# Performance work log

Measured on AMD Instinct MI355X. Metric: run time of the kernel, lower is better.

Reference implementation:

```python
import jax, jax.numpy as jnp
import numpy as np

N_TARGETS = 4
BATCH_SIZE = 4
B = N_TARGETS * BATCH_SIZE
N_SAMPLES = 1024
LAYERS = [(128, 128), (256, 64), (512, 32)]  # (channels, spatial)
EPS_COS = 1e-10


def setup_inputs() -> dict:
    key = jax.random.key(0)
    inp = {}
    for l, (c, s) in enumerate(LAYERS):
        k1, k2, k3, k4, key = jax.random.split(key, 5)
        n = s * s
        inp[f't{l}'] = jax.random.normal(k1, (N_TARGETS, c, s, s), dtype=jnp.float32)
        inp[f'g{l}'] = jax.random.normal(k2, (B, c, s, s), dtype=jnp.float32)
        inp[f'ix{l}'] = jax.random.randint(k3, (B, N_SAMPLES), 0, n)
        inp[f'iy{l}'] = jax.random.randint(k4, (B, N_SAMPLES), 0, n)
    return inp


def _cos_remd(x, y):
    # x: (b,n,c), y: (b,m,c)
    xn = jnp.linalg.norm(x, axis=2, keepdims=True)            # (b,n,1)
    yn = jnp.linalg.norm(y, axis=2, keepdims=True)            # (b,m,1)
    cross = jnp.einsum('bnc,bmc->bnm', x, y)                  # (b,n,m)
    dist = 1.0 - cross / (xn * yn.transpose(0, 2, 1) + EPS_COS)
    m1 = dist.min(axis=1).mean(axis=1)                        # min over n, mean over m
    m2 = dist.min(axis=2).mean(axis=1)                        # min over m, mean over n
    return jnp.maximum(m1, m2)                                # (b,)


def _moment_loss(x, y):
    mu_x = x.mean(axis=1, keepdims=True)
    mu_y = y.mean(axis=1, keepdims=True)
    mu_diff = jnp.abs(mu_x - mu_y).mean(axis=(1, 2))
    x_c = x - mu_x
    y_c = y - mu_y
    x_cov = jnp.einsum('bnc,bnd->bcd', x_c, x_c) / (x.shape[1] - 1)
    y_cov = jnp.einsum('bmc,bmd->bcd', y_c, y_c) / (y.shape[1] - 1)
    cov_diff = jnp.abs(x_cov - y_cov).mean(axis=(1, 2))
    return mu_diff + cov_diff                                 # (b,)


def _layer_loss(t, g, ix, iy):
    b, c, h, w = g.shape
    y = jnp.tile(t, (BATCH_SIZE, 1, 1, 1)).reshape(b, t.shape[1], -1)  # (b,c,n_y)
    x = g.reshape(b, c, -1)                                            # (b,c,n_x)
    x = jnp.take_along_axis(x, ix[:, None, :], axis=2)                 # (b,c,ns)
    y = jnp.take_along_axis(y, iy[:, None, :], axis=2)                 # (b,c,ns)
    x = x.transpose(0, 2, 1)
    y = y.transpose(0, 2, 1)
    return _cos_remd(x, y) + _moment_loss(x, y)


def reference(t0, g0, t1, g1, t2, g2, ix0, iy0, ix1, iy1, ix2, iy2):
    loss = (_layer_loss(t0, g0, ix0, iy0)
            + _layer_loss(t1, g1, ix1, iy1)
            + _layer_loss(t2, g2, ix2, iy2))
    return loss.reshape(BATCH_SIZE, N_TARGETS).mean(axis=0)   # (n_targets,)
```

## Files before the change

kernel.cpp:

```cpp
#include <hip/hip_runtime.h>
#include <math.h>

#define NT 4
#define BSZ 4
#define BB 16
#define NS 1024
#define GCH 4096
#define MAXL 3

typedef unsigned short u16;
typedef __attribute__((ext_vector_type(8))) short bf16x8;
typedef __attribute__((ext_vector_type(4))) float f32x4;

struct LayerP {
    const float *g, *t;
    const int *ix, *iy;
    u16 *Xt, *Yt, *Xs, *Ys;
    float *xp, *yp;
    float *rxn, *ryn;
    float *sx, *sy;
    unsigned *m1u, *m2u;
    float *cov;
    int C, n, nchunk, ntri, lid;
};
struct Tab {
    LayerP L[MAXL];
    int nl, nb, b0, ysh;
    float* losspart;
};

__device__ __forceinline__ unsigned fenc(float f) {
    unsigned u = __float_as_uint(f);
    return (u & 0x80000000u) ? ~u : (u | 0x80000000u);
}
__device__ __forceinline__ float fdec(unsigned u) {
    unsigned v = (u & 0x80000000u) ? (u & 0x7FFFFFFFu) : ~u;
    return __uint_as_float(v);
}
__device__ __forceinline__ u16 f2bf(float f) {
    unsigned u = __float_as_uint(f);
    unsigned r = u + 0x7FFFu + ((u >> 16) & 1u);
    return (u16)(r >> 16);
}
__device__ __forceinline__ float bf2f(u16 h) {
    return __uint_as_float((unsigned)h << 16);
}

__global__ __launch_bounds__(256) void gather_x(Tab tab)
{
    int x = blockIdx.x, l = 0;
    while (l < MAXL - 1 && x >= tab.L[l].C) { x -= tab.L[l].C; ++l; }
    const LayerP P = tab.L[l];
    int c = x, bl = blockIdx.y, bg = tab.b0 + bl;
    int tid = threadIdx.x;
    const float* __restrict__ grow = P.g + ((size_t)bg * P.C + c) * P.n;
    const int* __restrict__ ixr = P.ix + bg * NS;
    __shared__ __align__(16) float buf[GCH];
    __shared__ float red[4];
    int px[4];
    float xv[4] = {0.f, 0.f, 0.f, 0.f};
    #pragma unroll
    for (int r = 0; r < 4; ++r) px[r] = ixr[tid + r * 256];
    int n = P.n;
    for (int lo = 0; lo < n; lo += GCH) {
        int sz = min(GCH, n - lo);
        __syncthreads();
        for (int i = tid * 4; i < sz; i += 1024)
            *(float4*)&buf[i] = *(const float4*)&grow[lo + i];
        __syncthreads();
        #pragma unroll
        for (int r = 0; r < 4; ++r) {
            int rel = px[r] - lo;
            if ((unsigned)rel < (unsigned)sz) xv[r] = buf[rel];
        }
    }
    u16* __restrict__ xo = P.Xt + ((size_t)bl * P.C + c) * NS;
    float ax = 0.f;
    #pragma unroll
    for (int r = 0; r < 4; ++r) {
        u16 hb = f2bf(xv[r]);
        xo[tid + r * 256] = hb;
        ax += bf2f(hb);
    }
    for (int o = 32; o > 0; o >>= 1) ax += __shfl_down(ax, o);
    int wid = tid >> 6, lane = tid & 63;
    if (lane == 0) red[wid] = ax;
    __syncthreads();
    if (tid == 0) P.sx[bl * P.C + c] = red[0] + red[1] + red[2] + red[3];
}

__global__ __launch_bounds__(256) void gather_y(Tab tab)
{
    int x = blockIdx.x, l = 0;
    while (l < MAXL - 1 && x >= tab.L[l].C) { x -= tab.L[l].C; ++l; }
    const LayerP P = tab.L[l];
    int c = x, grp = blockIdx.y;
    int tid = threadIdx.x;
    int nk, tgt, bls[4];
    if (tab.ysh == NT) {
        nk = 4; tgt = grp;
        #pragma unroll
        for (int k = 0; k < 4; ++k) bls[k] = grp + NT * k;
    } else {
        nk = 1; bls[0] = grp; tgt = (tab.b0 + grp) % NT;
        bls[1] = bls[2] = bls[3] = 0;
    }
    const float* __restrict__ trow = P.t + ((size_t)tgt * P.C + c) * P.n;
    __shared__ __align__(16) float buf[GCH];
    __shared__ float red[4][4];
    int py[4][4];
    float yv[4][4];
    #pragma unroll
    for (int k = 0; k < 4; ++k) {
        if (k < nk) {
            const int* iyr = P.iy + (tab.b0 + bls[k]) * NS;
            #pragma unroll
            for (int r = 0; r < 4; ++r) { py[k][r] = iyr[tid + r * 256]; yv[k][r] = 0.f; }
        }
    }
    int n = P.n;
    for (int lo = 0; lo < n; lo += GCH) {
        int sz = min(GCH, n - lo);
        __syncthreads();
        for (int i = tid * 4; i < sz; i += 1024)
            *(float4*)&buf[i] = *(const float4*)&trow[lo + i];
        __syncthreads();
        #pragma unroll
        for (int k = 0; k < 4; ++k)
            if (k < nk) {
                #pragma unroll
                for (int r = 0; r < 4; ++r) {
                    int rel = py[k][r] - lo;
                    if ((unsigned)rel < (unsigned)sz) yv[k][r] = buf[rel];
                }
            }
    }
    int wid = tid >> 6, lane = tid & 63;
    #pragma unroll
    for (int k = 0; k < 4; ++k) {
        if (k >= nk) break;
        u16* __restrict__ yo = P.Yt + ((size_t)bls[k] * P.C + c) * NS;
        float ay = 0.f;
        #pragma unroll
        for (int r = 0; r < 4; ++r) {
            u16 hb = f2bf(yv[k][r]);
            yo[tid + r * 256] = hb;
            ay += bf2f(hb);
        }
        for (int o = 32; o > 0; o >>= 1) ay += __shfl_down(ay, o);
        if (lane == 0) red[k][wid] = ay;
    }
    __syncthreads();
    if (tid < nk)
        P.sy[bls[tid] * P.C + c] = red[tid][0] + red[tid][1] + red[tid][2] + red[tid][3];
}

__global__ void transpose_k(Tab tab)
{
    int x = blockIdx.x, l = 0;
    while (l < MAXL - 1 && x >= tab.L[l].C / 64) { x -= tab.L[l].C / 64; ++l; }
    const LayerP P = tab.L[l];
    int z = blockIdx.z;
    int bl = z >> 1, which = z & 1;
    const u16* __restrict__ Zt = which ? P.Yt : P.Xt;
    u16* __restrict__ Zs = which ? P.Ys : P.Xs;
    float* __restrict__ zp = which ? P.yp : P.xp;
    int C = P.C;
    int ctile = x;
    int c0 = ctile * 64, s0 = blockIdx.y * 64;
    __shared__ __align__(16) u16 T[64][72];
    int tid = threadIdx.x;
    #pragma unroll
    for (int rep = 0; rep < 2; ++rep) {
        int q = tid + rep * 256;
        int rr = q >> 3, seg = q & 7;
        *(float4*)&T[rr][seg * 8] =
            *(const float4*)&Zt[((size_t)bl * C + c0 + rr) * NS + s0 + seg * 8];
    }
    __syncthreads();
    #pragma unroll
    for (int rep = 0; rep < 2; ++rep) {
        int q = tid + rep * 256;
        int sr = q >> 3, cs = q & 7;
        __align__(16) u16 tmp[8];
        float p = 0.f;
        #pragma unroll
        for (int e = 0; e < 8; ++e) {
            u16 h = T[cs * 8 + e][sr];
            tmp[e] = h;
            float v = bf2f(h);
            p = fmaf(v, v, p);
        }
        *(float4*)&Zs[((size_t)bl * NS + s0 + sr) * C + c0 + cs * 8] = *(float4*)tmp;
        p += __shfl_xor(p, 1);
        p += __shfl_xor(p, 2);
        p += __shfl_xor(p, 4);
        if (cs == 0)
            zp[((size_t)bl * P.nchunk + ctile) * NS + s0 + sr] = p;
    }
}

__global__ void colnorm_reduce(Tab tab)
{
    const LayerP P = tab.L[blockIdx.y];
    int bl = blockIdx.z;
    int s = blockIdx.x * 256 + threadIdx.x;
    float ax = 0.f, ay = 0.f;
    for (int k = 0; k < P.nchunk; ++k) {
        size_t o = ((size_t)bl * P.nchunk + k) * NS + s;
        ax += P.xp[o];
        ay += P.yp[o];
    }
    P.rxn[bl * NS + s] = rsqrtf(ax);
    P.ryn[bl * NS + s] = rsqrtf(ay);
    P.m1u[bl * NS + s] = 0xFFFFFFFFu;
    P.m2u[bl * NS + s] = 0xFFFFFFFFu;
}

__global__ __launch_bounds__(256) void cross_mfma(Tab tab)
{
    int z = blockIdx.z;
    int l = z / tab.nb, bl = z - l * tab.nb;
    const LayerP P = tab.L[l];
    int C = P.C;
    int i0 = blockIdx.x * 128, j0 = blockIdx.y * 128;
    __shared__ __align__(16) u16 As[128][40], Bs[128][40];
    int tid = threadIdx.x;
    int w = tid >> 6, lane = tid & 63;
    int wr = w >> 1, wc = w & 1;
    int q = lane >> 4, r = lane & 15;
    const u16* __restrict__ Xb = P.Xs + ((size_t)bl * NS + i0) * C;
    const u16* __restrict__ Yb = P.Ys + ((size_t)bl * NS + j0) * C;
    f32x4 acc[4][4];
    #pragma unroll
    for (int m = 0; m < 4; ++m)
        #pragma unroll
        for (int nn = 0; nn < 4; ++nn) acc[m][nn] = (f32x4){0.f, 0.f, 0.f, 0.f};

    for (int kk = 0; kk < C; kk += 32) {
        __syncthreads();
        #pragma unroll
        for (int rep = 0; rep < 2; ++rep) {
            int qid = tid + rep * 256;
            int row = qid >> 2, seg = qid & 3;
            size_t off = (size_t)row * C + kk + seg * 8;
            *(float4*)&As[row][seg * 8] = *(const float4*)&Xb[off];
            *(float4*)&Bs[row][seg * 8] = *(const float4*)&Yb[off];
        }
        __syncthreads();
        bf16x8 a[4], b[4];
        #pragma unroll
        for (int m = 0; m < 4; ++m)
            a[m] = *(const bf16x8*)&As[wr * 64 + m * 16 + r][q * 8];
        #pragma unroll
        for (int nn = 0; nn < 4; ++nn)
            b[nn] = *(const bf16x8*)&Bs[wc * 64 + nn * 16 + r][q * 8];
        #pragma unroll
        for (int m = 0; m < 4; ++m)
            #pragma unroll
            for (int nn = 0; nn < 4; ++nn)
                acc[m][nn] = __builtin_amdgcn_mfma_f32_16x16x32_bf16(a[m], b[nn], acc[m][nn], 0, 0, 0);
    }

    float rxl[4][4], ryl[4];
    #pragma unroll
    for (int m = 0; m < 4; ++m)
        #pragma unroll
        for (int reg = 0; reg < 4; ++reg)
            rxl[m][reg] = P.rxn[bl * NS + i0 + wr * 64 + m * 16 + q * 4 + reg];
    #pragma unroll
    for (int nn = 0; nn < 4; ++nn)
        ryl[nn] = P.ryn[bl * NS + j0 + wc * 64 + nn * 16 + r];

    float rm[4][4], cm[4];
    #pragma unroll
    for (int m = 0; m < 4; ++m)
        #pragma unroll
        for (int reg = 0; reg < 4; ++reg) rm[m][reg] = 1e30f;
    #pragma unroll
    for (int nn = 0; nn < 4; ++nn) cm[nn] = 1e30f;
    #pragma unroll
    for (int m = 0; m < 4; ++m)
        #pragma unroll
        for (int nn = 0; nn < 4; ++nn)
            #pragma unroll
            for (int reg = 0; reg < 4; ++reg) {
                float d = 1.f - acc[m][nn][reg] * rxl[m][reg] * ryl[nn];
                rm[m][reg] = fminf(rm[m][reg], d);
                cm[nn] = fminf(cm[nn], d);
            }
    #pragma unroll
    for (int m = 0; m < 4; ++m)
        #pragma unroll
        for (int reg = 0; reg < 4; ++reg) {
            float v = rm[m][reg];
            v = fminf(v, __shfl_xor(v, 1));
            v = fminf(v, __shfl_xor(v, 2));
            v = fminf(v, __shfl_xor(v, 4));
            v = fminf(v, __shfl_xor(v, 8));
            rm[m][reg] = v;
        }
    if (r == 0) {
        #pragma unroll
        for (int m = 0; m < 4; ++m)
            #pragma unroll
            for (int reg = 0; reg < 4; ++reg) {
                int i = i0 + wr * 64 + m * 16 + q * 4 + reg;
                atomicMin(&P.m2u[bl * NS + i], fenc(rm[m][reg]));
            }
    }
    #pragma unroll
    for (int nn = 0; nn < 4; ++nn) {
        float v = cm[nn];
        v = fminf(v, __shfl_xor(v, 16));
        v = fminf(v, __shfl_xor(v, 32));
        cm[nn] = v;
    }
    if (q == 0) {
        #pragma unroll
        for (int nn = 0; nn < 4; ++nn) {
            int j = j0 + wc * 64 + nn * 16 + r;
            atomicMin(&P.m1u[bl * NS + j], fenc(cm[nn]));
        }
    }
}

__global__ __launch_bounds__(256) void cov_mfma(Tab tab)
{
    int x = blockIdx.x, l = 0;
    while (l < MAXL - 1 && x >= tab.L[l].ntri) { x -= tab.L[l].ntri; ++l; }
    const LayerP P = tab.L[l];
    int u = x;
    int bl = blockIdx.y;
    int C = P.C;
    int ty = 0;
    while ((ty + 1) * (ty + 2) / 2 <= u) ++ty;
    int tx = u - ty * (ty + 1) / 2;
    int c0 = ty * 128, d0 = tx * 128;
    float wgt = (tx == ty) ? 1.f : 2.f;

    __shared__ __align__(16) u16 As[128][40], Bs[128][40], Cs2[128][40], Ds[128][40];
    int tid = threadIdx.x;
    int w = tid >> 6, lane = tid & 63;
    int wr = w >> 1, wc = w & 1;
    int q = lane >> 4, r = lane & 15;
    const u16* __restrict__ Xc = P.Xt + ((size_t)bl * C + c0) * NS;
    const u16* __restrict__ Xd = P.Xt + ((size_t)bl * C + d0) * NS;
    const u16* __restrict__ Yc = P.Yt + ((size_t)bl * C + c0) * NS;
    const u16* __restrict__ Yd = P.Yt + ((size_t)bl * C + d0) * NS;

    f32x4 accX[4][4], accY[4][4];
    #pragma unroll
    for (int m = 0; m < 4; ++m)
        #pragma unroll
        for (int nn = 0; nn < 4; ++nn) {
            accX[m][nn] = (f32x4){0.f, 0.f, 0.f, 0.f};
            accY[m][nn] = (f32x4){0.f, 0.f, 0.f, 0.f};
        }

    for (int ss = 0; ss < NS; ss += 32) {
        __syncthreads();
        #pragma unroll
        for (int rep = 0; rep < 2; ++rep) {
            int qid = tid + rep * 256;
            int row = qid >> 2, seg = qid & 3;
            size_t off = (size_t)row * NS + ss + seg * 8;
            *(float4*)&As[row][seg * 8]  = *(const float4*)&Xc[off];
            *(float4*)&Bs[row][seg * 8]  = *(const float4*)&Xd[off];
            *(float4*)&Cs2[row][seg * 8] = *(const float4*)&Yc[off];
            *(float4*)&Ds[row][seg * 8]  = *(const float4*)&Yd[off];
        }
        __syncthreads();
        {
            bf16x8 a[4], b[4];
            #pragma unroll
            for (int m = 0; m < 4; ++m) a[m] = *(const bf16x8*)&As[wr * 64 + m * 16 + r][q * 8];
            #pragma unroll
            for (int nn = 0; nn < 4; ++nn) b[nn] = *(const bf16x8*)&Bs[wc * 64 + nn * 16 + r][q * 8];
            #pragma unroll
            for (int m = 0; m < 4; ++m)
                #pragma unroll
                for (int nn = 0; nn < 4; ++nn)
                    accX[m][nn] = __builtin_amdgcn_mfma_f32_16x16x32_bf16(a[m], b[nn], accX[m][nn], 0, 0, 0);
        }
        {
            bf16x8 a[4], b[4];
            #pragma unroll
            for (int m = 0; m < 4; ++m) a[m] = *(const bf16x8*)&Cs2[wr * 64 + m * 16 + r][q * 8];
            #pragma unroll
            for (int nn = 0; nn < 4; ++nn) b[nn] = *(const bf16x8*)&Ds[wc * 64 + nn * 16 + r][q * 8];
            #pragma unroll
            for (int m = 0; m < 4; ++m)
                #pragma unroll
                for (int nn = 0; nn < 4; ++nn)
                    accY[m][nn] = __builtin_amdgcn_mfma_f32_16x16x32_bf16(a[m], b[nn], accY[m][nn], 0, 0, 0);
        }
    }

    float scxv[4][4], scyv[4][4], sdxv[4], sdyv[4];
    #pragma unroll
    for (int m = 0; m < 4; ++m)
        #pragma unroll
        for (int reg = 0; reg < 4; ++reg) {
            int c = c0 + wr * 64 + m * 16 + q * 4 + reg;
            scxv[m][reg] = P.sx[bl * C + c];
            scyv[m][reg] = P.sy[bl * C + c];
        }
    #pragma unroll
    for (int nn = 0; nn < 4; ++nn) {
        int d = d0 + wc * 64 + nn * 16 + r;
        sdxv[nn] = P.sx[bl * C + d];
        sdyv[nn] = P.sy[bl * C + d];
    }
    const float invNS = 1.f / NS, invNSm1 = 1.f / (NS - 1);
    float tsum = 0.f;
    #pragma unroll
    for (int m = 0; m < 4; ++m)
        #pragma unroll
        for (int nn = 0; nn < 4; ++nn)
            #pragma unroll
            for (int reg = 0; reg < 4; ++reg) {
                float cx = (accX[m][nn][reg] - scxv[m][reg] * sdxv[nn] * invNS) * invNSm1;
                float cy = (accY[m][nn][reg] - scyv[m][reg] * sdyv[nn] * invNS) * invNSm1;
                tsum += fabsf(cx - cy);
            }
    tsum *= wgt;
    __shared__ float redc[4];
    for (int o = 32; o > 0; o >>= 1) tsum += __shfl_down(tsum, o);
    if (lane == 0) redc[w] = tsum;
    __syncthreads();
    if (tid == 0)
        P.cov[(size_t)bl * P.ntri + u] = redc[0] + redc[1] + redc[2] + redc[3];
}

__global__ void finalize_kernel(Tab tab)
{
    const LayerP P = tab.L[blockIdx.x];
    int bl = blockIdx.y;
    int tid = threadIdx.x;
    int C = P.C;
    float s1 = 0.f, s2 = 0.f, smu = 0.f, scov = 0.f;
    for (int s = tid; s < NS; s += 256) {
        s1 += fdec(P.m1u[bl * NS + s]);
        s2 += fdec(P.m2u[bl * NS + s]);
    }
    for (int c = tid; c < C; c += 256) smu += fabsf(P.sx[bl * C + c] - P.sy[bl * C + c]);
    for (int i = tid; i < P.ntri; i += 256) scov += P.cov[(size_t)bl * P.ntri + i];
    __shared__ float red[4][4];
    for (int o = 32; o > 0; o >>= 1) {
        s1 += __shfl_down(s1, o);
        s2 += __shfl_down(s2, o);
        smu += __shfl_down(smu, o);
        scov += __shfl_down(scov, o);
    }
    int wid = tid >> 6, lane = tid & 63;
    if (lane == 0) { red[0][wid] = s1; red[1][wid] = s2; red[2][wid] = smu; red[3][wid] = scov; }
    __syncthreads();
    if (tid == 0) {
        s1 = red[0][0] + red[0][1] + red[0][2] + red[0][3];
        s2 = red[1][0] + red[1][1] + red[1][2] + red[1][3];
        smu = red[2][0] + red[2][1] + red[2][2] + red[2][3];
        scov = red[3][0] + red[3][1] + red[3][2] + red[3][3];
        float m1m = s1 * (1.f / NS), m2m = s2 * (1.f / NS);
        float mu_diff = smu * (1.f / NS) * (1.f / (float)C);
        float cov_diff = scov / ((float)C * (float)C);
        tab.losspart[(tab.b0 + bl) * 3 + P.lid] = fmaxf(m1m, m2m) + mu_diff + cov_diff;
    }
}

__global__ void out_kernel(const float* __restrict__ lp, float* __restrict__ out)
{
    int t = threadIdx.x;
    if (t < NT) {
        float s = 0.f;
        for (int k = 0; k < BSZ; ++k)
            for (int l = 0; l < 3; ++l)
                s += lp[(k * NT + t) * 3 + l];
        out[t] = s * (1.f / BSZ);
    }
}

static inline size_t alignup(size_t v) { return (v + 255) & ~(size_t)255; }

static size_t layer_bytes(int C, int nb) {
    int nchunk = C / 64;
    int tc = C / 128, ntri = tc * (tc + 1) / 2;
    size_t szZ = alignup((size_t)NS * C * 2);
    size_t szP = alignup((size_t)nchunk * NS * 4);
    return (size_t)nb * (4 * szZ + 2 * szP + 4 * alignup(NS * 4)
                         + 2 * alignup(C * 4) + alignup(ntri * 4));
}

static char* fill_layer(LayerP& P, char* p, int C, int n, int nb, int lid,
                        const float* g, const float* t, const int* ix, const int* iy) {
    P.g = g; P.t = t; P.ix = ix; P.iy = iy;
    P.C = C; P.n = n; P.lid = lid;
    P.nchunk = C / 64;
    int tc = C / 128;
    P.ntri = tc * (tc + 1) / 2;
    size_t szZ = alignup((size_t)NS * C * 2);
    size_t szP = alignup((size_t)P.nchunk * NS * 4);
    P.Xt = (u16*)p;  p += nb * szZ;
    P.Yt = (u16*)p;  p += nb * szZ;
    P.Xs = (u16*)p;  p += nb * szZ;
    P.Ys = (u16*)p;  p += nb * szZ;
    P.xp = (float*)p; p += nb * szP;
    P.yp = (float*)p; p += nb * szP;
    P.rxn = (float*)p; p += nb * alignup(NS * 4);
    P.ryn = (float*)p; p += nb * alignup(NS * 4);
    P.m1u = (unsigned*)p; p += nb * alignup(NS * 4);
    P.m2u = (unsigned*)p; p += nb * alignup(NS * 4);
    P.sx = (float*)p; p += nb * alignup(C * 4);
    P.sy = (float*)p; p += nb * alignup(C * 4);
    P.cov = (float*)p; p += nb * alignup(P.ntri * 4);
    return p;
}

static void launch_group(const Tab& tab, hipStream_t stream) {
    int sumC = 0, sumC64 = 0, sumNtri = 0;
    for (int l = 0; l < tab.nl; ++l) {
        sumC += tab.L[l].C;
        sumC64 += tab.L[l].C / 64;
        sumNtri += tab.L[l].ntri;
    }
    int nb = tab.nb;
    int ygrid = (tab.ysh == NT) ? NT : nb;
    gather_x<<<dim3(sumC, nb), 256, 0, stream>>>(tab);
    gather_y<<<dim3(sumC, ygrid), 256, 0, stream>>>(tab);
    transpose_k<<<dim3(sumC64, NS / 64, nb * 2), 256, 0, stream>>>(tab);
    colnorm_reduce<<<dim3(NS / 256, tab.nl, nb), 256, 0, stream>>>(tab);
    cross_mfma<<<dim3(NS / 128, NS / 128, tab.nl * nb), 256, 0, stream>>>(tab);
    cov_mfma<<<dim3(sumNtri, nb), 256, 0, stream>>>(tab);
    finalize_kernel<<<dim3(tab.nl, nb), 256, 0, stream>>>(tab);
}

extern "C" void kernel_launch(void* const* d_in, const int* in_sizes, int n_in,
                              void* d_out, int out_size, void* d_ws, size_t ws_size,
                              hipStream_t stream)
{
    const float* tp[3] = {(const float*)d_in[0], (const float*)d_in[4], (const float*)d_in[8]};
    const float* gp[3] = {(const float*)d_in[1], (const float*)d_in[5], (const float*)d_in[9]};
    const int* ixp[3]  = {(const int*)d_in[2], (const int*)d_in[6], (const int*)d_in[10]};
    const int* iyp[3]  = {(const int*)d_in[3], (const int*)d_in[7], (const int*)d_in[11]};
    const int Cs[3] = {128, 256, 512};
    const int Sp[3] = {128, 64, 32};

    float* out = (float*)d_out;
    char* ws = (char*)d_ws;
    float* losspart = (float*)ws;
    size_t base = alignup(BB * 3 * 4);
    size_t avail = (ws_size > base) ? ws_size - base : 0;

    size_t need_all = 0;
    for (int l = 0; l < 3; ++l) need_all += layer_bytes(Cs[l], BB);

    if (avail >= need_all) {
        Tab tab;
        tab.nl = 3; tab.nb = BB; tab.b0 = 0; tab.ysh = NT; tab.losspart = losspart;
        char* p = ws + base;
        for (int l = 0; l < 3; ++l)
            p = fill_layer(tab.L[l], p, Cs[l], Sp[l] * Sp[l], BB, l,
                           gp[l], tp[l], ixp[l], iyp[l]);
        launch_group(tab, stream);
    } else {
        for (int l = 0; l < 3; ++l) {
            size_t per_b = layer_bytes(Cs[l], 1);
            int G = (int)(avail / per_b);
            if (G > BB) G = BB;
            if (G < 1) G = 1;
            for (int b0 = 0; b0 < BB; b0 += G) {
                int nb = (BB - b0 < G) ? (BB - b0) : G;
                Tab tab;
                tab.nl = 1; tab.nb = nb; tab.b0 = b0; tab.ysh = 1; tab.losspart = losspart;
                fill_layer(tab.L[0], ws + base, Cs[l], Sp[l] * Sp[l], nb, l,
                           gp[l], tp[l], ixp[l], iyp[l]);
                launch_group(tab, stream);
            }
        }
    }
    out_kernel<<<1, 64, 0, stream>>>(losspart, out);
}
```

Baseline: 230.5 us.

## Pipeline gather row loads via async global-to-LDS quad buffering

The gather kernels now stream each feature row into shared memory in 1024-float chunks with global_load_lds, keeping up to three chunks in flight in a four-slot ring buffer. Previously each 4096-float chunk was loaded synchronously between two full barriers. The aim is to overlap memory latency with the index lookups and to avoid the register round trip. The code assumes n is a multiple of 1024, which holds for these layers (16384, 4096, 1024), and it relies on precise vmcnt waits together with raw s_barrier.

```diff
diff --git a/kernel.cpp b/kernel.cpp
--- a/kernel.cpp
+++ b/kernel.cpp
@@ -5,7 +5,8 @@
 #define BSZ 4
 #define BB 16
 #define NS 1024
-#define GCH 4096
+#define CHF 1024
+#define NBUF 4
 #define MAXL 3
 
 typedef unsigned short u16;
@@ -46,6 +47,17 @@
     return __uint_as_float((unsigned)h << 16);
 }
 
+__device__ __forceinline__ void gload16(const float* src, float* dst) {
+    __builtin_amdgcn_global_load_lds(
+        (const __attribute__((address_space(1))) float*)src,
+        (__attribute__((address_space(3))) float*)dst, 16, 0, 0);
+}
+__device__ __forceinline__ void wait_rem(int rem) {
+    if (rem >= 2)      asm volatile("s_waitcnt vmcnt(2)" ::: "memory");
+    else if (rem == 1) asm volatile("s_waitcnt vmcnt(1)" ::: "memory");
+    else               asm volatile("s_waitcnt vmcnt(0)" ::: "memory");
+}
+
 __global__ __launch_bounds__(256) void gather_x(Tab tab)
 {
     int x = blockIdx.x, l = 0;
@@ -53,25 +65,31 @@
     const LayerP P = tab.L[l];
     int c = x, bl = blockIdx.y, bg = tab.b0 + bl;
     int tid = threadIdx.x;
+    int wv = tid >> 6, lane = tid & 63;
     const float* __restrict__ grow = P.g + ((size_t)bg * P.C + c) * P.n;
     const int* __restrict__ ixr = P.ix + bg * NS;
-    __shared__ __align__(16) float buf[GCH];
+    __shared__ __align__(16) float buf[NBUF][CHF];
     __shared__ float red[4];
     int px[4];
     float xv[4] = {0.f, 0.f, 0.f, 0.f};
     #pragma unroll
     for (int r = 0; r < 4; ++r) px[r] = ixr[tid + r * 256];
-    int n = P.n;
-    for (int lo = 0; lo < n; lo += GCH) {
-        int sz = min(GCH, n - lo);
-        __syncthreads();
-        for (int i = tid * 4; i < sz; i += 1024)
-            *(float4*)&buf[i] = *(const float4*)&grow[lo + i];
-        __syncthreads();
+    int nch = P.n >> 10;
+    int npro = nch < 3 ? nch : 3;
+    for (int d = 0; d < npro; ++d)
+        gload16(grow + d * CHF + wv * 256 + lane * 4, &buf[d][wv * 256]);
+    for (int ch = 0; ch < nch; ++ch) {
+        int rem = nch - 1 - ch; if (rem > 2) rem = 2;
+        wait_rem(rem);
+        __builtin_amdgcn_s_barrier();
+        __builtin_amdgcn_sched_barrier(0);
+        if (ch + 3 < nch)
+            gload16(grow + (ch + 3) * CHF + wv * 256 + lane * 4, &buf[(ch + 3) & 3][wv * 256]);
+        int lo = ch * CHF;
         #pragma unroll
         for (int r = 0; r < 4; ++r) {
             int rel = px[r] - lo;
-            if ((unsigned)rel < (unsigned)sz) xv[r] = buf[rel];
+            if ((unsigned)rel < (unsigned)CHF) xv[r] = buf[ch & 3][rel];
         }
     }
     u16* __restrict__ xo = P.Xt + ((size_t)bl * P.C + c) * NS;
@@ -83,8 +101,7 @@
         ax += bf2f(hb);
     }
     for (int o = 32; o > 0; o >>= 1) ax += __shfl_down(ax, o);
-    int wid = tid >> 6, lane = tid & 63;
-    if (lane == 0) red[wid] = ax;
+    if (lane == 0) red[wv] = ax;
     __syncthreads();
     if (tid == 0) P.sx[bl * P.C + c] = red[0] + red[1] + red[2] + red[3];
 }
@@ -96,6 +113,7 @@
     const LayerP P = tab.L[l];
     int c = x, grp = blockIdx.y;
     int tid = threadIdx.x;
+    int wv = tid >> 6, lane = tid & 63;
     int nk, tgt, bls[4];
     if (tab.ysh == NT) {
         nk = 4; tgt = grp;
@@ -106,7 +124,7 @@
         bls[1] = bls[2] = bls[3] = 0;
     }
     const float* __restrict__ trow = P.t + ((size_t)tgt * P.C + c) * P.n;
-    __shared__ __align__(16) float buf[GCH];
+    __shared__ __align__(16) float buf[NBUF][CHF];
     __shared__ float red[4][4];
     int py[4][4];
     float yv[4][4];
@@ -118,24 +136,28 @@
             for (int r = 0; r < 4; ++r) { py[k][r] = iyr[tid + r * 256]; yv[k][r] = 0.f; }
         }
     }
-    int n = P.n;
-    for (int lo = 0; lo < n; lo += GCH) {
-        int sz = min(GCH, n - lo);
-        __syncthreads();
-        for (int i = tid * 4; i < sz; i += 1024)
-            *(float4*)&buf[i] = *(const float4*)&trow[lo + i];
-        __syncthreads();
+    int nch = P.n >> 10;
+    int npro = nch < 3 ? nch : 3;
+    for (int d = 0; d < npro; ++d)
+        gload16(trow + d * CHF + wv * 256 + lane * 4, &buf[d][wv * 256]);
+    for (int ch = 0; ch < nch; ++ch) {
+        int rem = nch - 1 - ch; if (rem > 2) rem = 2;
+        wait_rem(rem);
+        __builtin_amdgcn_s_barrier();
+        __builtin_amdgcn_sched_barrier(0);
+        if (ch + 3 < nch)
+            gload16(trow + (ch + 3) * CHF + wv * 256 + lane * 4, &buf[(ch + 3) & 3][wv * 256]);
+        int lo = ch * CHF;
         #pragma unroll
         for (int k = 0; k < 4; ++k)
             if (k < nk) {
                 #pragma unroll
                 for (int r = 0; r < 4; ++r) {
                     int rel = py[k][r] - lo;
-                    if ((unsigned)rel < (unsigned)sz) yv[k][r] = buf[rel];
+                    if ((unsigned)rel < (unsigned)CHF) yv[k][r] = buf[ch & 3][rel];
                 }
             }
     }
-    int wid = tid >> 6, lane = tid & 63;
     #pragma unroll
     for (int k = 0; k < 4; ++k) {
         if (k >= nk) break;
@@ -148,7 +170,7 @@
             ay += bf2f(hb);
         }
         for (int o = 32; o > 0; o >>= 1) ay += __shfl_down(ay, o);
-        if (lane == 0) red[k][wid] = ay;
+        if (lane == 0) red[k][wv] = ay;
     }
     __syncthreads();
     if (tid < nk)
```

Result: slower. 238.3 us (+3.4%).

## Replace staged full-row gathers with direct per-sample gathers, move channel sums to transpose

Applied to the files above, without the earlier changes.

The two gather kernels used to stream each full channel row of g and t through shared memory and then pick out the sampled points. They are replaced by one flat-grid kernel where each thread loads its sampled index and reads 64 channels directly from global memory (a strided, uncoalesced gather). This avoids reading the whole feature map. The per-channel sums that gather used to compute now come from partial sums written by transpose_k and reduced in colnorm_reduce. The risk is scattered global reads with little coalescing, and the target-sharing across the batch is lost, so t values are re-read for each batch element.

```diff
diff --git a/kernel.cpp b/kernel.cpp
--- a/kernel.cpp
+++ b/kernel.cpp
@@ -5,7 +5,6 @@
 #define BSZ 4
 #define BB 16
 #define NS 1024
-#define GCH 4096
 #define MAXL 3
 
 typedef unsigned short u16;
@@ -17,15 +16,16 @@
     const int *ix, *iy;
     u16 *Xt, *Yt, *Xs, *Ys;
     float *xp, *yp;
+    float *xcs, *ycs;
     float *rxn, *ryn;
     float *sx, *sy;
     unsigned *m1u, *m2u;
     float *cov;
-    int C, n, nchunk, ntri, lid;
+    int C, n, nchunk, ntri, lid, xblk, yblk;
 };
 struct Tab {
     LayerP L[MAXL];
-    int nl, nb, b0, ysh;
+    int nl, nb, b0;
     float* losspart;
 };
 
@@ -46,113 +46,39 @@
     return __uint_as_float((unsigned)h << 16);
 }
 
-__global__ __launch_bounds__(256) void gather_x(Tab tab)
-{
-    int x = blockIdx.x, l = 0;
-    while (l < MAXL - 1 && x >= tab.L[l].C) { x -= tab.L[l].C; ++l; }
+__global__ __launch_bounds__(256) void gather(Tab tab)
+{
+    int f = blockIdx.x;
+    int l = 0, side = 0;
+    #pragma unroll
+    for (int li = 0; li < MAXL; ++li) {
+        if (li >= tab.nl) break;
+        if (f < tab.L[li].xblk) { l = li; side = 0; goto decoded; }
+        f -= tab.L[li].xblk;
+        if (f < tab.L[li].yblk) { l = li; side = 1; goto decoded; }
+        f -= tab.L[li].yblk;
+    }
+decoded:;
     const LayerP P = tab.L[l];
-    int c = x, bl = blockIdx.y, bg = tab.b0 + bl;
+    int ng = P.C >> 6;
+    int cgi = f % ng; f /= ng;
+    int sq = f & 3; f >>= 2;
+    int bl = f;
+    int bg = tab.b0 + bl;
+    int c0 = cgi * 64;
     int tid = threadIdx.x;
-    const float* __restrict__ grow = P.g + ((size_t)bg * P.C + c) * P.n;
-    const int* __restrict__ ixr = P.ix + bg * NS;
-    __shared__ __align__(16) float buf[GCH];
-    __shared__ float red[4];
-    int px[4];
-    float xv[4] = {0.f, 0.f, 0.f, 0.f};
-    #pragma unroll
-    for (int r = 0; r < 4; ++r) px[r] = ixr[tid + r * 256];
+    int s = sq * 256 + tid;
     int n = P.n;
-    for (int lo = 0; lo < n; lo += GCH) {
-        int sz = min(GCH, n - lo);
-        __syncthreads();
-        for (int i = tid * 4; i < sz; i += 1024)
-            *(float4*)&buf[i] = *(const float4*)&grow[lo + i];
-        __syncthreads();
-        #pragma unroll
-        for (int r = 0; r < 4; ++r) {
-            int rel = px[r] - lo;
-            if ((unsigned)rel < (unsigned)sz) xv[r] = buf[rel];
-        }
-    }
-    u16* __restrict__ xo = P.Xt + ((size_t)bl * P.C + c) * NS;
-    float ax = 0.f;
-    #pragma unroll
-    for (int r = 0; r < 4; ++r) {
-        u16 hb = f2bf(xv[r]);
-        xo[tid + r * 256] = hb;
-        ax += bf2f(hb);
-    }
-    for (int o = 32; o > 0; o >>= 1) ax += __shfl_down(ax, o);
-    int wid = tid >> 6, lane = tid & 63;
-    if (lane == 0) red[wid] = ax;
-    __syncthreads();
-    if (tid == 0) P.sx[bl * P.C + c] = red[0] + red[1] + red[2] + red[3];
-}
-
-__global__ __launch_bounds__(256) void gather_y(Tab tab)
-{
-    int x = blockIdx.x, l = 0;
-    while (l < MAXL - 1 && x >= tab.L[l].C) { x -= tab.L[l].C; ++l; }
-    const LayerP P = tab.L[l];
-    int c = x, grp = blockIdx.y;
-    int tid = threadIdx.x;
-    int nk, tgt, bls[4];
-    if (tab.ysh == NT) {
-        nk = 4; tgt = grp;
-        #pragma unroll
-        for (int k = 0; k < 4; ++k) bls[k] = grp + NT * k;
-    } else {
-        nk = 1; bls[0] = grp; tgt = (tab.b0 + grp) % NT;
-        bls[1] = bls[2] = bls[3] = 0;
-    }
-    const float* __restrict__ trow = P.t + ((size_t)tgt * P.C + c) * P.n;
-    __shared__ __align__(16) float buf[GCH];
-    __shared__ float red[4][4];
-    int py[4][4];
-    float yv[4][4];
-    #pragma unroll
-    for (int k = 0; k < 4; ++k) {
-        if (k < nk) {
-            const int* iyr = P.iy + (tab.b0 + bls[k]) * NS;
-            #pragma unroll
-            for (int r = 0; r < 4; ++r) { py[k][r] = iyr[tid + r * 256]; yv[k][r] = 0.f; }
-        }
-    }
-    int n = P.n;
-    for (int lo = 0; lo < n; lo += GCH) {
-        int sz = min(GCH, n - lo);
-        __syncthreads();
-        for (int i = tid * 4; i < sz; i += 1024)
-            *(float4*)&buf[i] = *(const float4*)&trow[lo + i];
-        __syncthreads();
-        #pragma unroll
-        for (int k = 0; k < 4; ++k)
-            if (k < nk) {
-                #pragma unroll
-                for (int r = 0; r < 4; ++r) {
-                    int rel = py[k][r] - lo;
-                    if ((unsigned)rel < (unsigned)sz) yv[k][r] = buf[rel];
-                }
-            }
-    }
-    int wid = tid >> 6, lane = tid & 63;
-    #pragma unroll
-    for (int k = 0; k < 4; ++k) {
-        if (k >= nk) break;
-        u16* __restrict__ yo = P.Yt + ((size_t)bls[k] * P.C + c) * NS;
-        float ay = 0.f;
-        #pragma unroll
-        for (int r = 0; r < 4; ++r) {
-            u16 hb = f2bf(yv[k][r]);
-            yo[tid + r * 256] = hb;
-            ay += bf2f(hb);
-        }
-        for (int o = 32; o > 0; o >>= 1) ay += __shfl_down(ay, o);
-        if (lane == 0) red[k][wid] = ay;
-    }
-    __syncthreads();
-    if (tid < nk)
-        P.sy[bls[tid] * P.C + c] = red[tid][0] + red[tid][1] + red[tid][2] + red[tid][3];
+    int idx = side ? P.iy[bg * NS + s] : P.ix[bg * NS + s];
+    const float* __restrict__ src =
+        (side ? P.t + ((size_t)(bg % NT) * P.C + c0) * n
+              : P.g + ((size_t)bg * P.C + c0) * n) + idx;
+    u16* __restrict__ dst = (side ? P.Yt : P.Xt) + ((size_t)bl * P.C + c0) * NS + s;
+    float v[64];
+    #pragma unroll
+    for (int j = 0; j < 64; ++j) v[j] = src[(size_t)j * n];
+    #pragma unroll
+    for (int j = 0; j < 64; ++j) dst[(size_t)j * NS] = f2bf(v[j]);
 }
 
 __global__ void transpose_k(Tab tab)
@@ -165,17 +91,28 @@
     const u16* __restrict__ Zt = which ? P.Yt : P.Xt;
     u16* __restrict__ Zs = which ? P.Ys : P.Xs;
     float* __restrict__ zp = which ? P.yp : P.xp;
+    float* __restrict__ zcs = which ? P.ycs : P.xcs;
     int C = P.C;
     int ctile = x;
     int c0 = ctile * 64, s0 = blockIdx.y * 64;
+    int stile = blockIdx.y;
     __shared__ __align__(16) u16 T[64][72];
     int tid = threadIdx.x;
     #pragma unroll
     for (int rep = 0; rep < 2; ++rep) {
         int q = tid + rep * 256;
         int rr = q >> 3, seg = q & 7;
-        *(float4*)&T[rr][seg * 8] =
-            *(const float4*)&Zt[((size_t)bl * C + c0 + rr) * NS + s0 + seg * 8];
+        float4 f4 = *(const float4*)&Zt[((size_t)bl * C + c0 + rr) * NS + s0 + seg * 8];
+        *(float4*)&T[rr][seg * 8] = f4;
+        const u16* hp = (const u16*)&f4;
+        float p = 0.f;
+        #pragma unroll
+        for (int e = 0; e < 8; ++e) p += bf2f(hp[e]);
+        p += __shfl_xor(p, 1);
+        p += __shfl_xor(p, 2);
+        p += __shfl_xor(p, 4);
+        if (seg == 0)
+            zcs[(((size_t)bl * P.nchunk + ctile) * 16 + stile) * 64 + rr] = p;
     }
     __syncthreads();
     #pragma unroll
@@ -215,6 +152,18 @@
     P.ryn[bl * NS + s] = rsqrtf(ay);
     P.m1u[bl * NS + s] = 0xFFFFFFFFu;
     P.m2u[bl * NS + s] = 0xFFFFFFFFu;
+    int cq = P.C >> 2;
+    for (int c = blockIdx.x * cq + threadIdx.x; c < (blockIdx.x + 1) * cq; c += 256) {
+        int ct = c >> 6, cr = c & 63;
+        float sx = 0.f, sy = 0.f;
+        for (int st = 0; st < 16; ++st) {
+            size_t o = (((size_t)bl * P.nchunk + ct) * 16 + st) * 64 + cr;
+            sx += P.xcs[o];
+            sy += P.ycs[o];
+        }
+        P.sx[bl * P.C + c] = sx;
+        P.sy[bl * P.C + c] = sy;
+    }
 }
 
 __global__ __launch_bounds__(256) void cross_mfma(Tab tab)
@@ -482,13 +431,15 @@
 
 static inline size_t alignup(size_t v) { return (v + 255) & ~(size_t)255; }
 
-static size_t layer_bytes(int C, int nb) {
+static size_t layer_bytes(int C, int n, int nb) {
     int nchunk = C / 64;
     int tc = C / 128, ntri = tc * (tc + 1) / 2;
     size_t szZ = alignup((size_t)NS * C * 2);
     size_t szP = alignup((size_t)nchunk * NS * 4);
+    size_t szCS = alignup((size_t)nb * nchunk * 16 * 64 * 4);
     return (size_t)nb * (4 * szZ + 2 * szP + 4 * alignup(NS * 4)
-                         + 2 * alignup(C * 4) + alignup(ntri * 4));
+                         + 2 * alignup(C * 4) + alignup(ntri * 4))
+           + 2 * szCS;
 }
 
 static char* fill_layer(LayerP& P, char* p, int C, int n, int nb, int lid,
@@ -498,14 +449,19 @@
     P.nchunk = C / 64;
     int tc = C / 128;
     P.ntri = tc * (tc + 1) / 2;
+    P.xblk = (C / 64) * 4 * nb;
+    P.yblk = (C / 64) * 4 * nb;
     size_t szZ = alignup((size_t)NS * C * 2);
     size_t szP = alignup((size_t)P.nchunk * NS * 4);
+    size_t szCS = alignup((size_t)nb * P.nchunk * 16 * 64 * 4);
     P.Xt = (u16*)p;  p += nb * szZ;
     P.Yt = (u16*)p;  p += nb * szZ;
     P.Xs = (u16*)p;  p += nb * szZ;
     P.Ys = (u16*)p;  p += nb * szZ;
     P.xp = (float*)p; p += nb * szP;
     P.yp = (float*)p; p += nb * szP;
+    P.xcs = (float*)p; p += szCS;
+    P.ycs = (float*)p; p += szCS;
     P.rxn = (float*)p; p += nb * alignup(NS * 4);
     P.ryn = (float*)p; p += nb * alignup(NS * 4);
     P.m1u = (unsigned*)p; p += nb * alignup(NS * 4);
@@ -517,16 +473,14 @@
 }
 
 static void launch_group(const Tab& tab, hipStream_t stream) {
-    int sumC = 0, sumC64 = 0, sumNtri = 0;
+    int sumC64 = 0, sumNtri = 0, flatN = 0;
     for (int l = 0; l < tab.nl; ++l) {
-        sumC += tab.L[l].C;
         sumC64 += tab.L[l].C / 64;
         sumNtri += tab.L[l].ntri;
+        flatN += tab.L[l].xblk + tab.L[l].yblk;
     }
     int nb = tab.nb;
-    int ygrid = (tab.ysh == NT) ? NT : nb;
-    gather_x<<<dim3(sumC, nb), 256, 0, stream>>>(tab);
-    gather_y<<<dim3(sumC, ygrid), 256, 0, stream>>>(tab);
+    gather<<<flatN, 256, 0, stream>>>(tab);
     transpose_k<<<dim3(sumC64, NS / 64, nb * 2), 256, 0, stream>>>(tab);
     colnorm_reduce<<<dim3(NS / 256, tab.nl, nb), 256, 0, stream>>>(tab);
     cross_mfma<<<dim3(NS / 128, NS / 128, tab.nl * nb), 256, 0, stream>>>(tab);
@@ -552,11 +506,11 @@
     size_t avail = (ws_size > base) ? ws_size - base : 0;
 
     size_t need_all = 0;
-    for (int l = 0; l < 3; ++l) need_all += layer_bytes(Cs[l], BB);
+    for (int l = 0; l < 3; ++l) need_all += layer_bytes(Cs[l], Sp[l] * Sp[l], BB);
 
     if (avail >= need_all) {
         Tab tab;
-        tab.nl = 3; tab.nb = BB; tab.b0 = 0; tab.ysh = NT; tab.losspart = losspart;
+        tab.nl = 3; tab.nb = BB; tab.b0 = 0; tab.losspart = losspart;
         char* p = ws + base;
         for (int l = 0; l < 3; ++l)
             p = fill_layer(tab.L[l], p, Cs[l], Sp[l] * Sp[l], BB, l,
@@ -564,14 +518,14 @@
         launch_group(tab, stream);
     } else {
         for (int l = 0; l < 3; ++l) {
-            size_t per_b = layer_bytes(Cs[l], 1);
+            size_t per_b = layer_bytes(Cs[l], Sp[l] * Sp[l], 1);
             int G = (int)(avail / per_b);
             if (G > BB) G = BB;
             if (G < 1) G = 1;
             for (int b0 = 0; b0 < BB; b0 += G) {
                 int nb = (BB - b0 < G) ? (BB - b0) : G;
                 Tab tab;
-                tab.nl = 1; tab.nb = nb; tab.b0 = b0; tab.ysh = 1; tab.losspart = losspart;
+                tab.nl = 1; tab.nb = nb; tab.b0 = b0; tab.losspart = losspart;
                 fill_layer(tab.L[0], ws + base, Cs[l], Sp[l] * Sp[l], nb, l,
                            gp[l], tp[l], ixp[l], iyp[l]);
                 launch_group(tab, stream);
```

After: 276.6 us. 20.0% more time.
